# Kernel tuning notes

Measured on AMD Instinct MI355X. Metric: run time of the kernel, lower is better.

## Reference

```python
import jax, jax.numpy as jnp
import numpy as np
from functools import partial

H = 768
E = 1536
B = 4
L = 4096

def layer_norm(x, g, b, eps=1e-5):
    mu = jnp.mean(x, axis=-1, keepdims=True)
    var = jnp.mean((x - mu) ** 2, axis=-1, keepdims=True)
    return (x - mu) * jax.lax.rsqrt(var + eps) * g + b

def l2_normalize(x, eps=1e-12):
    n = jnp.sqrt(jnp.sum(x * x, axis=-1, keepdims=True))
    return x / jnp.maximum(n, eps)

def dw_conv(x, w):
    # x: [B, L, E], w: [E, 1, 3] depthwise kernel (torch Conv1d groups=E layout)
    y = jax.lax.conv_general_dilated(
        x.transpose(0, 2, 1), w, window_strides=(1,), padding=[(1, 1)],
        dimension_numbers=('NCH', 'OIH', 'NCH'), feature_group_count=E)
    return y.transpose(0, 2, 1)

def setup_inputs() -> dict:
    key = jax.random.key(0)
    ks = jax.random.split(key, 12)
    d = {}
    d['x'] = jax.random.normal(ks[0], (B, L, H), jnp.float32)
    d['ln1_g'] = jnp.ones((H,), jnp.float32)
    d['ln1_b'] = jnp.zeros((H,), jnp.float32)
    d['ln2_g'] = jnp.ones((E,), jnp.float32)
    d['ln2_b'] = jnp.zeros((E,), jnp.float32)
    d['W_in'] = 0.02 * jax.random.normal(ks[1], (3 * E, H), jnp.float32)
    d['b_in'] = jnp.zeros((3 * E,), jnp.float32)
    d['W_beta'] = jnp.zeros((E, H), jnp.float32)  # torch init: constant 0
    d['b_beta'] = jnp.ones((E,), jnp.float32)     # torch init: constant 1
    d['W_out'] = 0.02 * jax.random.normal(ks[2], (H, E), jnp.float32)
    d['b_out'] = jnp.zeros((H,), jnp.float32)
    d['W1'] = 0.02 * jax.random.normal(ks[3], (4 * H, H), jnp.float32)
    d['b1'] = jnp.zeros((4 * H,), jnp.float32)
    d['W2'] = 0.02 * jax.random.normal(ks[4], (H, 4 * H), jnp.float32)
    d['b2'] = jnp.zeros((H,), jnp.float32)
    d['conv_w'] = jax.random.normal(ks[5], (E, 1, 3), jnp.float32) / jnp.sqrt(3.0)
    d['attn_scale'] = jnp.ones((1,), jnp.float32)
    return d

def reference(x, ln1_g, ln1_b, ln2_g, ln2_b, W_in, b_in, W_beta, b_beta,
              W_out, b_out, W1, b1, W2, b2, conv_w, attn_scale):
    shortcut = x
    xn = layer_norm(x, ln1_g, ln1_b)
    qkv = xn @ W_in.T + b_in
    q, k, v = jnp.split(qkv, 3, axis=-1)
    q = jax.nn.silu(q)
    k = jax.nn.silu(k)
    v = jax.nn.gelu(v, approximate=False)
    q = l2_normalize(q) + 0.1 * k
    k = l2_normalize(k) + 0.1 * q
    q = dw_conv(q, conv_w)
    k = dw_conv(k, conv_w)
    v = dw_conv(v, conv_w)
    beta = jax.nn.sigmoid(xn @ W_beta.T + b_beta) * 0.9 + 0.1
    # initial state is zero, so v_old = 0 and v_new = beta * v (same math as torch code)
    v_new = beta * v                                   # [B, L, E]
    state = jnp.einsum('ble,blf->bef', v_new, k)       # v_new^T @ k : [B, E, E]
    out = jnp.einsum('blf,bef->ble', q, state)         # q @ state^T
    out = out * attn_scale
    out = layer_norm(out, ln2_g, ln2_b)
    out = out @ W_out.T + b_out
    x = shortcut + out
    h = layer_norm(x, ln1_g, ln1_b)
    h = jax.nn.gelu(h @ W1.T + b1, approximate=False) @ W2.T + b2
    return x + h
```

## Files before the change

### kernel.cpp

```cpp
#include <hip/hip_runtime.h>
#include <hip/hip_bf16.h>
#include <cstdint>
#include <cstddef>

using bf16_t = __hip_bfloat16;
typedef __bf16 bf16x8 __attribute__((ext_vector_type(8)));
typedef __bf16 bf16x4 __attribute__((ext_vector_type(4)));
typedef float f32x4 __attribute__((ext_vector_type(4)));

#define DEVI static __device__ __forceinline__

DEVI float b2f(bf16_t v) { return __bfloat162float(v); }

DEVI float fsigmoid(float x) { return 1.0f / (1.0f + __expf(-x)); }
DEVI float fsilu(float x) { return x * fsigmoid(x); }

DEVI float ferf(float x) {
    const float ax = fabsf(x);
    const float t = 1.0f / fmaf(0.3275911f, ax, 1.0f);
    float p = fmaf(1.061405429f, t, -1.453152027f);
    p = fmaf(p, t, 1.421413741f);
    p = fmaf(p, t, -0.284496736f);
    p = fmaf(p, t, 0.254829592f);
    p = p * t * __expf(-ax * ax);
    return copysignf(1.0f - p, x);
}
DEVI float fgelu(float x) { return 0.5f * x * (1.0f + ferf(x * 0.70710678118654752440f)); }

DEVI void g2l16(const bf16_t* g, bf16_t* l) {
    __builtin_amdgcn_global_load_lds(
        (const __attribute__((address_space(1))) void*)g,
        (__attribute__((address_space(3))) void*)l,
        16, 0, 0);
}

DEVI f32x4 mfma16(bf16x8 a, bf16x8 b, f32x4 c) {
    return __builtin_amdgcn_mfma_f32_16x16x32_bf16(a, b, c, 0, 0, 0);
}

template<int ACT, bool RESID, bool OUTBF, bool QKVSPLIT>
__global__ __launch_bounds__(256) void gemm_nt(
    const bf16_t* __restrict__ A, const bf16_t* __restrict__ B,
    void* __restrict__ Cout, const float* __restrict__ bias,
    const float* __restrict__ resid,
    float* __restrict__ normq, float* __restrict__ normk,
    int M, int N, int K, long long sA, long long sB, long long sC)
{
    __shared__ bf16_t As[128 * 64];
    __shared__ bf16_t Bs[128 * 64];

    const int t  = threadIdx.x;
    const int w  = t >> 6;
    const int ln = t & 63;
    const long long bz = blockIdx.z;
    A += bz * sA;
    B += bz * sB;
    const long long cbase = QKVSPLIT ? 0 : bz * sC;

    const int m0 = blockIdx.y * 128;
    const int n0 = blockIdx.x * 128;
    const int wm = (w >> 1) * 64;
    const int wn = (w & 1) * 64;

    f32x4 acc[4][4] = {};

    const int sr = ln >> 3;
    const int sc = (ln & 7) ^ sr;
    const bf16_t* Ap = A + (size_t)(m0 + w * 32 + sr) * K + sc * 8;
    const bf16_t* Bp = B + (size_t)(n0 + w * 32 + sr) * K + sc * 8;
    bf16_t* ldsA = &As[(w * 32) * 64];
    bf16_t* ldsB = &Bs[(w * 32) * 64];

    const int fr = ln & 15;
    const int qd = ln >> 4;
    int roA[4], roB[4];
#pragma unroll
    for (int i = 0; i < 4; ++i) {
        roA[i] = (wm + i * 16 + fr) * 64;
        roB[i] = (wn + i * 16 + fr) * 64;
    }
    const int so0 = ((qd)     ^ (fr & 7)) * 8;
    const int so1 = ((4 + qd) ^ (fr & 7)) * 8;

    for (int k0 = 0; k0 < K; k0 += 64) {
#pragma unroll
        for (int i = 0; i < 4; ++i) {
            g2l16(Ap + (size_t)(i * 8) * K, ldsA + (i * 8) * 64);
            g2l16(Bp + (size_t)(i * 8) * K, ldsB + (i * 8) * 64);
        }
        Ap += 64; Bp += 64;
        __syncthreads();

        bf16x8 af[4], bfr[4];
#pragma unroll
        for (int i = 0; i < 4; ++i) {
            af[i]  = *(const bf16x8*)&As[roA[i] + so0];
            bfr[i] = *(const bf16x8*)&Bs[roB[i] + so0];
        }
#pragma unroll
        for (int mi = 0; mi < 4; ++mi)
#pragma unroll
            for (int ni = 0; ni < 4; ++ni)
                acc[mi][ni] = mfma16(bfr[ni], af[mi], acc[mi][ni]);
#pragma unroll
        for (int i = 0; i < 4; ++i) {
            af[i]  = *(const bf16x8*)&As[roA[i] + so1];
            bfr[i] = *(const bf16x8*)&Bs[roB[i] + so1];
        }
#pragma unroll
        for (int mi = 0; mi < 4; ++mi)
#pragma unroll
            for (int ni = 0; ni < 4; ++ni)
                acc[mi][ni] = mfma16(bfr[ni], af[mi], acc[mi][ni]);
        __syncthreads();
    }

    const int rb = qd * 4;
    const int seg = QKVSPLIT ? (n0 / 1536) : 0;
    f32x4 bias4[4];
#pragma unroll
    for (int ni = 0; ni < 4; ++ni) {
        f32x4 z = {};
        bias4[ni] = bias ? *(const f32x4*)&bias[n0 + wn + ni * 16 + rb] : z;
    }
#pragma unroll
    for (int mi = 0; mi < 4; ++mi) {
        const int row = m0 + wm + mi * 16 + fr;
        float s2 = 0.f;
#pragma unroll
        for (int ni = 0; ni < 4; ++ni) {
            const int col0 = n0 + wn + ni * 16 + rb;
            f32x4 v = acc[mi][ni] + bias4[ni];
            if constexpr (ACT == 1) {
#pragma unroll
                for (int r = 0; r < 4; ++r) v[r] = fgelu(v[r]);
            }
            if constexpr (ACT == 3) {
                if (seg <= 1) {
#pragma unroll
                    for (int r = 0; r < 4; ++r) v[r] = fsilu(v[r]);
                    s2 += v[0]*v[0] + v[1]*v[1] + v[2]*v[2] + v[3]*v[3];
                } else if (seg == 2) {
#pragma unroll
                    for (int r = 0; r < 4; ++r) v[r] = fgelu(v[r]);
                } else {
#pragma unroll
                    for (int r = 0; r < 4; ++r) v[r] = fsigmoid(v[r]) * 0.9f + 0.1f;
                }
            }
            long long off;
            if constexpr (QKVSPLIT) {
                off = (long long)seg * sC + (long long)row * 1536
                    + (col0 - seg * 1536);
            } else {
                off = cbase + (long long)row * N + col0;
            }
            if constexpr (RESID) v += *(const f32x4*)&resid[off];
            if constexpr (OUTBF) {
                bf16x4 o;
#pragma unroll
                for (int r = 0; r < 4; ++r) o[r] = (__bf16)v[r];
                *(bf16x4*)((bf16_t*)Cout + off) = o;
            } else {
                *(f32x4*)((float*)Cout + off) = v;
            }
        }
        if constexpr (ACT == 3) {
            if (seg <= 1) {
                s2 += __shfl_xor(s2, 16, 64);
                s2 += __shfl_xor(s2, 32, 64);
                if (qd == 0)
                    atomicAdd((seg == 0 ? normq : normk) + row, s2);
            }
        }
    }
}

template<int ACT, bool RESID, bool OUTBF, bool QKVSPLIT>
__global__ __launch_bounds__(512) void gemm256(
    const bf16_t* __restrict__ A, const bf16_t* __restrict__ B,
    void* __restrict__ Cout, const float* __restrict__ bias,
    const float* __restrict__ resid,
    float* __restrict__ normq, float* __restrict__ normk,
    int M, int N, int K, long long sA, long long sB, long long sC)
{
    __shared__ bf16_t As[2][256 * 64];
    __shared__ bf16_t Bs[2][256 * 64];

    const int t  = threadIdx.x;
    const int w  = t >> 6;
    const int ln = t & 63;
    const int wr = w >> 2;
    const int wc = w & 3;
    const long long bz = blockIdx.z;
    A += bz * sA;
    B += bz * sB;
    const long long cbase = QKVSPLIT ? 0 : bz * sC;

    const int m0 = blockIdx.y * 256;
    const int n0 = blockIdx.x * 256;

    const int fr = ln & 15;
    const int qd = ln >> 4;
    const int sr = ln >> 3;
    const int scx = ((ln & 7) ^ sr) * 8;

    const bf16_t* gA[2];
    const bf16_t* gB[2];
    int lA[2], lB[2];
#pragma unroll
    for (int i = 0; i < 2; ++i) {
        const int b  = w * 2 + i;
        const int rA = ((b >> 3) << 7) + ((b & 7) << 3);
        const int rB = ((b >> 2) << 6) + ((b & 3) << 3);
        gA[i] = A + (size_t)(m0 + rA + sr) * K + scx;
        gB[i] = B + (size_t)(n0 + rB + sr) * K + scx;
        lA[i] = rA * 64;
        lB[i] = rB * 64;
    }
    const size_t K64 = (size_t)K * 64;
    const size_t K32 = (size_t)K * 32;
    const int NT = K >> 6;

    const int ck0 = ((qd)     ^ (fr & 7)) * 8;
    const int ck1 = ((4 + qd) ^ (fr & 7)) * 8;
    const int raB = (wr * 128 + fr) * 64;
    const int rbB = (wc * 64  + fr) * 64;

    f32x4 acc[8][4] = {};

#pragma unroll
    for (int i = 0; i < 2; ++i) {
        g2l16(gA[i],       &As[0][lA[i]]);
        g2l16(gA[i] + K64, &As[0][lA[i] + 4096]);
        g2l16(gB[i],       &Bs[0][lB[i]]);
        g2l16(gB[i] + K32, &Bs[0][lB[i] + 2048]);
    }
#pragma unroll
    for (int i = 0; i < 2; ++i) {
        g2l16(gB[i] + K32 + 64, &Bs[1][lB[i] + 2048]);
        g2l16(gA[i] + K64 + 64, &As[1][lA[i] + 4096]);
    }
    asm volatile("s_waitcnt vmcnt(4)" ::: "memory");
    __builtin_amdgcn_sched_barrier(0);
    __builtin_amdgcn_s_barrier();

    for (int u = 0; u < NT; ++u) {
        const int bs = u & 1;
        const bf16_t* Ac = As[bs];
        const bf16_t* Bc = Bs[bs];
        bf16_t* An  = As[bs ^ 1];
        bf16_t* Bn  = Bs[bs ^ 1];
        bf16_t* Acw = As[bs];
        bf16_t* Bcw = Bs[bs];
        const size_t kc1 = (size_t)(u + 1) * 64;
        const size_t kc2 = (size_t)(u + 2) * 64;
        const bool p1 = (u + 1) < NT;
        const bool p2 = (u + 2) < NT;

        bf16x8 a0[4][2], a1[4][2], bq0[2][2], bq1[2][2];

#pragma unroll
        for (int mi = 0; mi < 4; ++mi) {
            a0[mi][0] = *(const bf16x8*)&Ac[raB + mi * 1024 + ck0];
            a0[mi][1] = *(const bf16x8*)&Ac[raB + mi * 1024 + ck1];
        }
#pragma unroll
        for (int ni = 0; ni < 2; ++ni) {
            bq0[ni][0] = *(const bf16x8*)&Bc[rbB + ni * 1024 + ck0];
            bq0[ni][1] = *(const bf16x8*)&Bc[rbB + ni * 1024 + ck1];
        }
        if (p1) {
            g2l16(gA[0] + kc1, &An[lA[0]]);
            g2l16(gA[1] + kc1, &An[lA[1]]);
        }
        __builtin_amdgcn_s_barrier();
        asm volatile("s_waitcnt lgkmcnt(0)" ::: "memory");
        __builtin_amdgcn_sched_barrier(0);
        __builtin_amdgcn_s_setprio(1);
#pragma unroll
        for (int mi = 0; mi < 4; ++mi)
#pragma unroll
            for (int ni = 0; ni < 2; ++ni) {
                acc[mi][ni] = mfma16(bq0[ni][0], a0[mi][0], acc[mi][ni]);
                acc[mi][ni] = mfma16(bq0[ni][1], a0[mi][1], acc[mi][ni]);
            }
        __builtin_amdgcn_s_setprio(0);
        __builtin_amdgcn_sched_barrier(0);
        __builtin_amdgcn_s_barrier();

#pragma unroll
        for (int ni = 0; ni < 2; ++ni) {
            bq1[ni][0] = *(const bf16x8*)&Bc[rbB + 2048 + ni * 1024 + ck0];
            bq1[ni][1] = *(const bf16x8*)&Bc[rbB + 2048 + ni * 1024 + ck1];
        }
        if (p1) {
            g2l16(gB[0] + kc1, &Bn[lB[0]]);
            g2l16(gB[1] + kc1, &Bn[lB[1]]);
        }
        __builtin_amdgcn_s_barrier();
        asm volatile("s_waitcnt lgkmcnt(0)" ::: "memory");
        __builtin_amdgcn_sched_barrier(0);
        __builtin_amdgcn_s_setprio(1);
#pragma unroll
        for (int mi = 0; mi < 4; ++mi)
#pragma unroll
            for (int ni = 0; ni < 2; ++ni) {
                acc[mi][ni + 2] = mfma16(bq1[ni][0], a0[mi][0], acc[mi][ni + 2]);
                acc[mi][ni + 2] = mfma16(bq1[ni][1], a0[mi][1], acc[mi][ni + 2]);
            }
        __builtin_amdgcn_s_setprio(0);
        __builtin_amdgcn_sched_barrier(0);
        __builtin_amdgcn_s_barrier();

#pragma unroll
        for (int mi = 0; mi < 4; ++mi) {
            a1[mi][0] = *(const bf16x8*)&Ac[raB + 4096 + mi * 1024 + ck0];
            a1[mi][1] = *(const bf16x8*)&Ac[raB + 4096 + mi * 1024 + ck1];
        }
        if (p2) {
            g2l16(gB[0] + K32 + kc2, &Bcw[lB[0] + 2048]);
            g2l16(gB[1] + K32 + kc2, &Bcw[lB[1] + 2048]);
        }
        __builtin_amdgcn_s_barrier();
        asm volatile("s_waitcnt lgkmcnt(0)" ::: "memory");
        __builtin_amdgcn_sched_barrier(0);
        __builtin_amdgcn_s_setprio(1);
#pragma unroll
        for (int mi = 0; mi < 4; ++mi)
#pragma unroll
            for (int ni = 0; ni < 2; ++ni) {
                acc[mi + 4][ni] = mfma16(bq0[ni][0], a1[mi][0], acc[mi + 4][ni]);
                acc[mi + 4][ni] = mfma16(bq0[ni][1], a1[mi][1], acc[mi + 4][ni]);
            }
        __builtin_amdgcn_s_setprio(0);
        __builtin_amdgcn_sched_barrier(0);
        __builtin_amdgcn_s_barrier();

        if (p2) {
            g2l16(gA[0] + K64 + kc2, &Acw[lA[0] + 4096]);
            g2l16(gA[1] + K64 + kc2, &Acw[lA[1] + 4096]);
        }
        __builtin_amdgcn_s_setprio(1);
#pragma unroll
        for (int mi = 0; mi < 4; ++mi)
#pragma unroll
            for (int ni = 0; ni < 2; ++ni) {
                acc[mi + 4][ni + 2] = mfma16(bq1[ni][0], a1[mi][0], acc[mi + 4][ni + 2]);
                acc[mi + 4][ni + 2] = mfma16(bq1[ni][1], a1[mi][1], acc[mi + 4][ni + 2]);
            }
        __builtin_amdgcn_s_setprio(0);
        __builtin_amdgcn_sched_barrier(0);
        if (p2) asm volatile("s_waitcnt vmcnt(4)" ::: "memory");
        else    asm volatile("s_waitcnt vmcnt(0)" ::: "memory");
        __builtin_amdgcn_sched_barrier(0);
        __builtin_amdgcn_s_barrier();
    }

    const int rb = qd * 4;
    const int seg = QKVSPLIT ? (n0 / 1536) : 0;
    f32x4 bias4[4];
#pragma unroll
    for (int ni = 0; ni < 4; ++ni) {
        f32x4 z = {};
        bias4[ni] = bias ? *(const f32x4*)&bias[n0 + wc * 64 + ni * 16 + rb] : z;
    }
#pragma unroll
    for (int mi = 0; mi < 8; ++mi) {
        const int row = m0 + wr * 128 + mi * 16 + fr;
        float s2 = 0.f;
#pragma unroll
        for (int ni = 0; ni < 4; ++ni) {
            const int col0 = n0 + wc * 64 + ni * 16 + rb;
            f32x4 v = acc[mi][ni] + bias4[ni];
            if constexpr (ACT == 1) {
#pragma unroll
                for (int r = 0; r < 4; ++r) v[r] = fgelu(v[r]);
            }
            if constexpr (ACT == 3) {
                if (seg <= 1) {
#pragma unroll
                    for (int r = 0; r < 4; ++r) v[r] = fsilu(v[r]);
                    s2 += v[0]*v[0] + v[1]*v[1] + v[2]*v[2] + v[3]*v[3];
                } else if (seg == 2) {
#pragma unroll
                    for (int r = 0; r < 4; ++r) v[r] = fgelu(v[r]);
                } else {
#pragma unroll
                    for (int r = 0; r < 4; ++r) v[r] = fsigmoid(v[r]) * 0.9f + 0.1f;
                }
            }
            long long off;
            if constexpr (QKVSPLIT) {
                off = (long long)seg * sC + (long long)row * 1536
                    + (col0 - seg * 1536);
            } else {
                off = cbase + (long long)row * N + col0;
            }
            if constexpr (RESID) v += *(const f32x4*)&resid[off];
            if constexpr (OUTBF) {
                bf16x4 o;
#pragma unroll
                for (int r = 0; r < 4; ++r) o[r] = (__bf16)v[r];
                *(bf16x4*)((bf16_t*)Cout + off) = o;
            } else {
                *(f32x4*)((float*)Cout + off) = v;
            }
        }
        if constexpr (ACT == 3) {
            if (seg <= 1) {
                s2 += __shfl_xor(s2, 16, 64);
                s2 += __shfl_xor(s2, 32, 64);
                if (qd == 0)
                    atomicAdd((seg == 0 ? normq : normk) + row, s2);
            }
        }
    }
}

template<int NT>
__global__ __launch_bounds__(NT) void ln_v4(
    const float* __restrict__ x, const float* __restrict__ g,
    const float* __restrict__ b, bf16_t* __restrict__ out)
{
    constexpr int n = NT * 4;
    constexpr int NW = NT / 64;
    const int row = blockIdx.x, t = threadIdx.x;
    f32x4 v = *(const f32x4*)&x[(size_t)row * n + t * 4];
    float s  = v[0] + v[1] + v[2] + v[3];
    float ss = v[0]*v[0] + v[1]*v[1] + v[2]*v[2] + v[3]*v[3];
#pragma unroll
    for (int m = 32; m; m >>= 1) { s += __shfl_xor(s, m, 64); ss += __shfl_xor(ss, m, 64); }
    __shared__ float red[2 * NW];
    const int w = t >> 6;
    if ((t & 63) == 0) { red[w] = s; red[NW + w] = ss; }
    __syncthreads();
    s = 0.f; ss = 0.f;
#pragma unroll
    for (int i = 0; i < NW; ++i) { s += red[i]; ss += red[NW + i]; }
    const float mean = s / n;
    const float rstd = rsqrtf(ss / n - mean * mean + 1e-5f);
    const f32x4 gv = *(const f32x4*)&g[t * 4];
    const f32x4 bv = *(const f32x4*)&b[t * 4];
    bf16x4 o;
#pragma unroll
    for (int r = 0; r < 4; ++r)
        o[r] = (__bf16)((v[r] - mean) * rstd * gv[r] + bv[r]);
    *(bf16x4*)&out[(size_t)row * n + t * 4] = o;
}

__global__ __launch_bounds__(192) void ln_bf16_1536(
    const bf16_t* __restrict__ x, const float* __restrict__ g,
    const float* __restrict__ b, bf16_t* __restrict__ out,
    const float* __restrict__ scale_ptr)
{
    const int row = blockIdx.x, t = threadIdx.x;
    const float scale = scale_ptr[0];
    const bf16x8 x8 = *(const bf16x8*)&x[(size_t)row * 1536 + t * 8];
    float v[8];
    float s = 0.f, ss = 0.f;
#pragma unroll
    for (int i = 0; i < 8; ++i) {
        v[i] = (float)x8[i] * scale;
        s += v[i]; ss += v[i] * v[i];
    }
#pragma unroll
    for (int m = 32; m; m >>= 1) { s += __shfl_xor(s, m, 64); ss += __shfl_xor(ss, m, 64); }
    __shared__ float red[6];
    const int w = t >> 6;
    if ((t & 63) == 0) { red[w] = s; red[3 + w] = ss; }
    __syncthreads();
    s  = red[0] + red[1] + red[2];
    ss = red[3] + red[4] + red[5];
    const float mean = s / 1536.f;
    const float rstd = rsqrtf(ss / 1536.f - mean * mean + 1e-5f);
    const f32x4 g0 = *(const f32x4*)&g[t * 8];
    const f32x4 g1 = *(const f32x4*)&g[t * 8 + 4];
    const f32x4 b0 = *(const f32x4*)&b[t * 8];
    const f32x4 b1 = *(const f32x4*)&b[t * 8 + 4];
    bf16x8 o;
#pragma unroll
    for (int r = 0; r < 4; ++r) {
        o[r]     = (__bf16)((v[r]     - mean) * rstd * g0[r] + b0[r]);
        o[r + 4] = (__bf16)((v[r + 4] - mean) * rstd * g1[r] + b1[r]);
    }
    *(bf16x8*)&out[(size_t)row * 1536 + t * 8] = o;
}

__global__ __launch_bounds__(256) void ac_qk(
    const bf16_t* __restrict__ qs, const bf16_t* __restrict__ ks,
    const float* __restrict__ nq, const float* __restrict__ nk,
    bf16_t* __restrict__ qc, bf16_t* __restrict__ kT,
    const float* __restrict__ cw)
{
    constexpr int L = 4096, E = 1536;
    const int b = blockIdx.z;
    const int e0 = blockIdx.x * 64, l0 = blockIdx.y * 64;
    const int t = threadIdx.x;
    const int e = e0 + (t & 15) * 4;
    const int lbase = l0 + (t >> 4) * 4;
    const size_t rowL = (size_t)b * L;

    float w0[4], w1[4], w2[4];
#pragma unroll
    for (int i = 0; i < 4; ++i) {
        w0[i] = cw[(e + i) * 3 + 0];
        w1[i] = cw[(e + i) * 3 + 1];
        w2[i] = cw[(e + i) * 3 + 2];
    }

    float sq[6][4], sk[6][4];
#pragma unroll
    for (int j = 0; j < 6; ++j) {
        const int l = lbase - 1 + j;
        if (l < 0 || l >= L) {
#pragma unroll
            for (int i = 0; i < 4; ++i) { sq[j][i] = 0.f; sk[j][i] = 0.f; }
            continue;
        }
        const size_t off = (rowL + l) * E + e;
        const bf16x4 q4 = *(const bf16x4*)&qs[off];
        const bf16x4 k4 = *(const bf16x4*)&ks[off];
        const float rq = 1.0f / fmaxf(sqrtf(nq[rowL + l]), 1e-12f);
        const float rk = 1.0f / fmaxf(sqrtf(nk[rowL + l]), 1e-12f);
#pragma unroll
        for (int i = 0; i < 4; ++i) {
            const float q1 = (float)q4[i] * rq + 0.1f * (float)k4[i];
            const float k1 = (float)k4[i] * rk + 0.1f * q1;
            sq[j][i] = q1; sk[j][i] = k1;
        }
    }

#pragma unroll
    for (int j = 0; j < 4; ++j) {
        bf16x4 oq;
#pragma unroll
        for (int i = 0; i < 4; ++i)
            oq[i] = (__bf16)(w0[i] * sq[j][i] + w1[i] * sq[j + 1][i] + w2[i] * sq[j + 2][i]);
        *(bf16x4*)&qc[(rowL + lbase + j) * E + e] = oq;
    }
#pragma unroll
    for (int i = 0; i < 4; ++i) {
        bf16x4 ok;
#pragma unroll
        for (int j = 0; j < 4; ++j)
            ok[j] = (__bf16)(w0[i] * sk[j][i] + w1[i] * sk[j + 1][i] + w2[i] * sk[j + 2][i]);
        *(bf16x4*)&kT[((size_t)b * E + e + i) * L + lbase] = ok;
    }
}

__global__ __launch_bounds__(256) void ac_v(
    const bf16_t* __restrict__ vg, const bf16_t* __restrict__ beta,
    bf16_t* __restrict__ vT, const float* __restrict__ cw)
{
    constexpr int L = 4096, E = 1536;
    const int b = blockIdx.z;
    const int e0 = blockIdx.x * 64, l0 = blockIdx.y * 64;
    const int t = threadIdx.x;
    const int e = e0 + (t & 15) * 4;
    const int lbase = l0 + (t >> 4) * 4;
    const size_t rowL = (size_t)b * L;

    float w0[4], w1[4], w2[4];
#pragma unroll
    for (int i = 0; i < 4; ++i) {
        w0[i] = cw[(e + i) * 3 + 0];
        w1[i] = cw[(e + i) * 3 + 1];
        w2[i] = cw[(e + i) * 3 + 2];
    }

    float s[6][4];
#pragma unroll
    for (int j = 0; j < 6; ++j) {
        const int l = lbase - 1 + j;
        if (l < 0 || l >= L) {
#pragma unroll
            for (int i = 0; i < 4; ++i) s[j][i] = 0.f;
            continue;
        }
        const bf16x4 v4 = *(const bf16x4*)&vg[(rowL + l) * E + e];
#pragma unroll
        for (int i = 0; i < 4; ++i) s[j][i] = (float)v4[i];
    }

    float o[4][4];
#pragma unroll
    for (int j = 0; j < 4; ++j) {
        const bf16x4 b4 = *(const bf16x4*)&beta[(rowL + lbase + j) * E + e];
#pragma unroll
        for (int i = 0; i < 4; ++i)
            o[j][i] = (w0[i] * s[j][i] + w1[i] * s[j + 1][i] + w2[i] * s[j + 2][i])
                      * (float)b4[i];
    }
#pragma unroll
    for (int i = 0; i < 4; ++i) {
        bf16x4 ov;
#pragma unroll
        for (int j = 0; j < 4; ++j) ov[j] = (__bf16)o[j][i];
        *(bf16x4*)&vT[((size_t)b * E + e + i) * L + lbase] = ov;
    }
}

__global__ __launch_bounds__(256) void prep1(
    const float* __restrict__ Win, const float* __restrict__ Wbeta,
    const float* __restrict__ bin, const float* __restrict__ bbeta,
    bf16_t* __restrict__ Wcat, float* __restrict__ bcat)
{
    constexpr int nWin4 = 3 * 1536 * 768 / 4;
    constexpr int nWb4  = 1536 * 768 / 4;
    const int i = blockIdx.x * 256 + threadIdx.x;
    if (i < nWin4) {
        const f32x4 v = ((const f32x4*)Win)[i];
        bf16x4 o;
#pragma unroll
        for (int r = 0; r < 4; ++r) o[r] = (__bf16)v[r];
        ((bf16x4*)Wcat)[i] = o;
    } else if (i < nWin4 + nWb4) {
        const f32x4 v = ((const f32x4*)Wbeta)[i - nWin4];
        bf16x4 o;
#pragma unroll
        for (int r = 0; r < 4; ++r) o[r] = (__bf16)v[r];
        ((bf16x4*)Wcat)[i] = o;
    } else {
        const int j = i - nWin4 - nWb4;
        ((f32x4*)bcat)[j] = (j < 1152) ? ((const f32x4*)bin)[j]
                                       : ((const f32x4*)bbeta)[j - 1152];
    }
}

__global__ __launch_bounds__(256) void prep2(
    const float* __restrict__ Wout, const float* __restrict__ W1,
    const float* __restrict__ W2, bf16_t* __restrict__ dst)
{
    constexpr int n0 = 768 * 1536 / 4;
    constexpr int n1 = n0 + 3072 * 768 / 4;
    const int i = blockIdx.x * 256 + threadIdx.x;
    const float* src;
    int j;
    if (i < n0)      { src = Wout; j = i; }
    else if (i < n1) { src = W1;   j = i - n0; }
    else             { src = W2;   j = i - n1; }
    const f32x4 v = ((const f32x4*)src)[j];
    bf16x4 o;
#pragma unroll
    for (int r = 0; r < 4; ++r) o[r] = (__bf16)v[r];
    ((bf16x4*)dst)[i] = o;
}

__global__ void diag_ws(float* o, float v) { o[threadIdx.x] = v; }


extern "C" void kernel_launch(void* const* d_in, const int* in_sizes, int n_in,
                              void* d_out, int out_size, void* d_ws, size_t ws_size,
                              hipStream_t stream)
{
    constexpr int B = 4, L = 4096, H = 768, E = 1536;
    constexpr int T = B * L;
    constexpr size_t SEGE = (size_t)T * E;
    constexpr size_t S    = SEGE * 2;
    constexpr size_t o_bcat  = 5 * S;
    constexpr size_t o_norms = o_bcat + 6144 * 4;
    constexpr size_t WS_NEED = o_norms + (size_t)T * 8;

    const float* x       = (const float*)d_in[0];
    const float* ln1_g   = (const float*)d_in[1];
    const float* ln1_b   = (const float*)d_in[2];
    const float* ln2_g   = (const float*)d_in[3];
    const float* ln2_b   = (const float*)d_in[4];
    const float* W_in    = (const float*)d_in[5];
    const float* b_in    = (const float*)d_in[6];
    const float* W_beta  = (const float*)d_in[7];
    const float* b_beta  = (const float*)d_in[8];
    const float* W_out   = (const float*)d_in[9];
    const float* b_out   = (const float*)d_in[10];
    const float* W1      = (const float*)d_in[11];
    const float* b1      = (const float*)d_in[12];
    const float* W2      = (const float*)d_in[13];
    const float* b2      = (const float*)d_in[14];
    const float* conv_w  = (const float*)d_in[15];
    const float* attn_sc = (const float*)d_in[16];

    if (ws_size < WS_NEED) {
        diag_ws<<<1, 256, 0, stream>>>((float*)d_out,
                                       10000.0f + (float)(ws_size >> 20));
        return;
    }

    char* ws = (char*)d_ws;
    bf16_t* slotA = (bf16_t*)(ws + 0 * S);
    bf16_t* slotB = (bf16_t*)(ws + 1 * S);
    bf16_t* slotC = (bf16_t*)(ws + 2 * S);
    bf16_t* slotD = (bf16_t*)(ws + 3 * S);
    bf16_t* slotE = (bf16_t*)(ws + 4 * S);
    float*  bcat  = (float*)(ws + o_bcat);
    float*  nq    = (float*)(ws + o_norms);
    float*  nk    = nq + T;

    bf16_t* Wcat = slotE;
    bf16_t* xn   = (bf16_t*)((char*)slotE + (size_t)6144 * H * 2);

    bf16_t* vT    = slotE;
    bf16_t* kT    = slotC;
    bf16_t* qc    = slotD;
    bf16_t* state = slotA;
    bf16_t* WoutB = (bf16_t*)((char*)slotA + (size_t)20 * 1024 * 1024);
    bf16_t* W1B   = WoutB + (size_t)H * E;
    bf16_t* W2B   = W1B + (size_t)4 * H * H;
    bf16_t* attn  = slotB;
    bf16_t* ln2o  = slotE;
    float*  x2    = (float*)slotC;
    bf16_t* xn2   = slotB;
    bf16_t* h1    = slotD;

    hipMemsetAsync(nq, 0, (size_t)T * 2 * sizeof(float), stream);
    prep1<<<4614, 256, 0, stream>>>(W_in, W_beta, b_in, b_beta, Wcat, bcat);

    ln_v4<192><<<T, 192, 0, stream>>>(x, ln1_g, ln1_b, xn);

    gemm256<3, false, true, true><<<dim3(6144 / 256, T / 256, 1), 512, 0, stream>>>(
        xn, Wcat, slotA, bcat, nullptr, nq, nk, T, 6144, H, 0, 0, (long long)SEGE);

    ac_v <<<dim3(E / 64, L / 64, B), 256, 0, stream>>>(slotC, slotD, vT, conv_w);
    ac_qk<<<dim3(E / 64, L / 64, B), 256, 0, stream>>>(slotA, slotB, nq, nk, qc, kT, conv_w);

    prep2<<<5760, 256, 0, stream>>>(W_out, W1, W2, WoutB);

    gemm_nt<0, false, true, false><<<dim3(E / 128, E / 128, B), 256, 0, stream>>>(
        vT, kT, state, nullptr, nullptr, nullptr, nullptr, E, E, L,
        (long long)E * L, (long long)E * L, (long long)E * E);

    gemm256<0, false, true, false><<<dim3(E / 256, L / 256, B), 512, 0, stream>>>(
        qc, state, attn, nullptr, nullptr, nullptr, nullptr, L, E, E,
        (long long)L * E, (long long)E * E, (long long)L * E);

    ln_bf16_1536<<<T, 192, 0, stream>>>(attn, ln2_g, ln2_b, ln2o, attn_sc);

    gemm_nt<0, true, false, false><<<dim3(H / 128, T / 128, 1), 256, 0, stream>>>(
        ln2o, WoutB, x2, b_out, x, nullptr, nullptr, T, H, E, 0, 0, 0);

    ln_v4<192><<<T, 192, 0, stream>>>(x2, ln1_g, ln1_b, xn2);

    gemm256<1, false, true, false><<<dim3(4 * H / 256, T / 256, 1), 512, 0, stream>>>(
        xn2, W1B, h1, b1, nullptr, nullptr, nullptr, T, 4 * H, H, 0, 0, 0);

    gemm_nt<0, true, false, false><<<dim3(H / 128, T / 128, 1), 256, 0, stream>>>(
        h1, W2B, (float*)d_out, b2, x2, nullptr, nullptr, T, H, 4 * H, 0, 0, 0);
}
```

Baseline: 1.001 ms.

## Switch 256x256 GEMM to 32x32x16 MFMA with register-prefetched LDS fragments

Rewrites the inner loop of the large-tile GEMM to use 32x32x16 bf16 MFMA instead of 16x16x32, cutting the number of MFMA issues and LDS fragment reads per tile. It also restructures the pipeline: fragments for the next k-slice are read from LDS into registers while the current slice's MFMAs run, and global-to-LDS staging becomes a simple double buffer, one tile ahead, with one barrier per k-tile. The epilogue is remapped to the 32x32 accumulator layout and needs only one shuffle for the row-norm reduction. Risks include higher register pressure from the 16-wide accumulators and less prefetch depth, because the vmcnt(0) wait now comes every iteration.

```diff
diff --git a/kernel.cpp b/kernel.cpp
--- a/kernel.cpp
+++ b/kernel.cpp
@@ -7,6 +7,7 @@
 typedef __bf16 bf16x8 __attribute__((ext_vector_type(8)));
 typedef __bf16 bf16x4 __attribute__((ext_vector_type(4)));
 typedef float f32x4 __attribute__((ext_vector_type(4)));
+typedef float f32x16 __attribute__((ext_vector_type(16)));
 
 #define DEVI static __device__ __forceinline__
 
@@ -36,6 +37,9 @@
 
 DEVI f32x4 mfma16(bf16x8 a, bf16x8 b, f32x4 c) {
     return __builtin_amdgcn_mfma_f32_16x16x32_bf16(a, b, c, 0, 0, 0);
+}
+DEVI f32x16 mfma32(bf16x8 a, bf16x8 b, f32x16 c) {
+    return __builtin_amdgcn_mfma_f32_32x32x16_bf16(a, b, c, 0, 0, 0);
 }
 
 template<int ACT, bool RESID, bool OUTBF, bool QKVSPLIT>
@@ -200,11 +204,8 @@
     const int m0 = blockIdx.y * 256;
     const int n0 = blockIdx.x * 256;
 
-    const int fr = ln & 15;
-    const int qd = ln >> 4;
     const int sr = ln >> 3;
     const int scx = ((ln & 7) ^ sr) * 8;
-
     const bf16_t* gA[2];
     const bf16_t* gB[2];
     int lA[2], lB[2];
@@ -222,196 +223,167 @@
     const size_t K32 = (size_t)K * 32;
     const int NT = K >> 6;
 
-    const int ck0 = ((qd)     ^ (fr & 7)) * 8;
-    const int ck1 = ((4 + qd) ^ (fr & 7)) * 8;
-    const int raB = (wr * 128 + fr) * 64;
-    const int rbB = (wc * 64  + fr) * 64;
-
-    f32x4 acc[8][4] = {};
-
-#pragma unroll
-    for (int i = 0; i < 2; ++i) {
-        g2l16(gA[i],       &As[0][lA[i]]);
-        g2l16(gA[i] + K64, &As[0][lA[i] + 4096]);
-        g2l16(gB[i],       &Bs[0][lB[i]]);
-        g2l16(gB[i] + K32, &Bs[0][lB[i] + 2048]);
-    }
-#pragma unroll
-    for (int i = 0; i < 2; ++i) {
-        g2l16(gB[i] + K32 + 64, &Bs[1][lB[i] + 2048]);
-        g2l16(gA[i] + K64 + 64, &As[1][lA[i] + 4096]);
-    }
-    asm volatile("s_waitcnt vmcnt(4)" ::: "memory");
+    const int lr = ln & 31;
+    const int hh = ln >> 5;
+    const int r7 = ln & 7;
+    int rowA[4], rowB[2], sl[4];
+#pragma unroll
+    for (int mi = 0; mi < 4; ++mi) rowA[mi] = (wr * 128 + mi * 32 + lr) * 64;
+#pragma unroll
+    for (int ni = 0; ni < 2; ++ni) rowB[ni] = (wc * 64 + ni * 32 + lr) * 64;
+#pragma unroll
+    for (int ks = 0; ks < 4; ++ks) sl[ks] = ((2 * ks + hh) ^ r7) * 8;
+
+    f32x16 acc[4][2];
+#pragma unroll
+    for (int mi = 0; mi < 4; ++mi)
+#pragma unroll
+        for (int ni = 0; ni < 2; ++ni)
+#pragma unroll
+            for (int r = 0; r < 16; ++r) acc[mi][ni][r] = 0.f;
+
+    bf16x8 fA0[4], fB0[2], fA1[4], fB1[2];
+
+#define STAGE_A(dst, kc) do { \
+    g2l16(gA[0] + (kc),       &(dst)[lA[0]]); \
+    g2l16(gA[0] + K64 + (kc), &(dst)[lA[0] + 4096]); \
+    g2l16(gA[1] + (kc),       &(dst)[lA[1]]); \
+    g2l16(gA[1] + K64 + (kc), &(dst)[lA[1] + 4096]); } while (0)
+#define STAGE_B(dst, kc) do { \
+    g2l16(gB[0] + (kc),       &(dst)[lB[0]]); \
+    g2l16(gB[0] + K32 + (kc), &(dst)[lB[0] + 2048]); \
+    g2l16(gB[1] + (kc),       &(dst)[lB[1]]); \
+    g2l16(gB[1] + K32 + (kc), &(dst)[lB[1] + 2048]); } while (0)
+#define RD6(fa, fb, Ab, Bb, slot) do { \
+    fa[0] = *(const bf16x8*)&(Ab)[rowA[0] + (slot)]; \
+    fa[1] = *(const bf16x8*)&(Ab)[rowA[1] + (slot)]; \
+    fa[2] = *(const bf16x8*)&(Ab)[rowA[2] + (slot)]; \
+    fa[3] = *(const bf16x8*)&(Ab)[rowA[3] + (slot)]; \
+    fb[0] = *(const bf16x8*)&(Bb)[rowB[0] + (slot)]; \
+    fb[1] = *(const bf16x8*)&(Bb)[rowB[1] + (slot)]; } while (0)
+#define MFMA8(fa, fb) do { \
+    __builtin_amdgcn_s_setprio(1); \
+    acc[0][0] = mfma32(fb[0], fa[0], acc[0][0]); \
+    acc[0][1] = mfma32(fb[1], fa[0], acc[0][1]); \
+    acc[1][0] = mfma32(fb[0], fa[1], acc[1][0]); \
+    acc[1][1] = mfma32(fb[1], fa[1], acc[1][1]); \
+    acc[2][0] = mfma32(fb[0], fa[2], acc[2][0]); \
+    acc[2][1] = mfma32(fb[1], fa[2], acc[2][1]); \
+    acc[3][0] = mfma32(fb[0], fa[3], acc[3][0]); \
+    acc[3][1] = mfma32(fb[1], fa[3], acc[3][1]); \
+    __builtin_amdgcn_s_setprio(0); } while (0)
+
+    STAGE_A(As[0], 0);
+    STAGE_B(Bs[0], 0);
+    asm volatile("s_waitcnt vmcnt(0)" ::: "memory");
     __builtin_amdgcn_sched_barrier(0);
     __builtin_amdgcn_s_barrier();
+    __builtin_amdgcn_sched_barrier(0);
+    RD6(fA0, fB0, As[0], Bs[0], sl[0]);
 
     for (int u = 0; u < NT; ++u) {
         const int bs = u & 1;
         const bf16_t* Ac = As[bs];
         const bf16_t* Bc = Bs[bs];
-        bf16_t* An  = As[bs ^ 1];
-        bf16_t* Bn  = Bs[bs ^ 1];
-        bf16_t* Acw = As[bs];
-        bf16_t* Bcw = Bs[bs];
+        bf16_t* An = As[bs ^ 1];
+        bf16_t* Bn = Bs[bs ^ 1];
         const size_t kc1 = (size_t)(u + 1) * 64;
-        const size_t kc2 = (size_t)(u + 2) * 64;
         const bool p1 = (u + 1) < NT;
-        const bool p2 = (u + 2) < NT;
-
-        bf16x8 a0[4][2], a1[4][2], bq0[2][2], bq1[2][2];
-
-#pragma unroll
-        for (int mi = 0; mi < 4; ++mi) {
-            a0[mi][0] = *(const bf16x8*)&Ac[raB + mi * 1024 + ck0];
-            a0[mi][1] = *(const bf16x8*)&Ac[raB + mi * 1024 + ck1];
-        }
-#pragma unroll
-        for (int ni = 0; ni < 2; ++ni) {
-            bq0[ni][0] = *(const bf16x8*)&Bc[rbB + ni * 1024 + ck0];
-            bq0[ni][1] = *(const bf16x8*)&Bc[rbB + ni * 1024 + ck1];
-        }
-        if (p1) {
-            g2l16(gA[0] + kc1, &An[lA[0]]);
-            g2l16(gA[1] + kc1, &An[lA[1]]);
-        }
-        __builtin_amdgcn_s_barrier();
+
+        if (p1) STAGE_A(An, kc1);
+        RD6(fA1, fB1, Ac, Bc, sl[1]);
+        asm volatile("s_waitcnt lgkmcnt(6)" ::: "memory");
+        __builtin_amdgcn_sched_barrier(0);
+        MFMA8(fA0, fB0);
+
+        if (p1) STAGE_B(Bn, kc1);
+        RD6(fA0, fB0, Ac, Bc, sl[2]);
+        asm volatile("s_waitcnt lgkmcnt(6)" ::: "memory");
+        __builtin_amdgcn_sched_barrier(0);
+        MFMA8(fA1, fB1);
+
+        RD6(fA1, fB1, Ac, Bc, sl[3]);
+        asm volatile("s_waitcnt lgkmcnt(6)" ::: "memory");
+        __builtin_amdgcn_sched_barrier(0);
+        MFMA8(fA0, fB0);
+
         asm volatile("s_waitcnt lgkmcnt(0)" ::: "memory");
         __builtin_amdgcn_sched_barrier(0);
-        __builtin_amdgcn_s_setprio(1);
-#pragma unroll
-        for (int mi = 0; mi < 4; ++mi)
-#pragma unroll
-            for (int ni = 0; ni < 2; ++ni) {
-                acc[mi][ni] = mfma16(bq0[ni][0], a0[mi][0], acc[mi][ni]);
-                acc[mi][ni] = mfma16(bq0[ni][1], a0[mi][1], acc[mi][ni]);
-            }
-        __builtin_amdgcn_s_setprio(0);
+        asm volatile("s_waitcnt vmcnt(0)" ::: "memory");
         __builtin_amdgcn_sched_barrier(0);
         __builtin_amdgcn_s_barrier();
-
+        __builtin_amdgcn_sched_barrier(0);
+        if (p1) RD6(fA0, fB0, An, Bn, sl[0]);
+        MFMA8(fA1, fB1);
+    }
+#undef STAGE_A
+#undef STAGE_B
+#undef RD6
+#undef MFMA8
+
+    const int h4 = hh * 4;
+    const int seg = QKVSPLIT ? (n0 / 1536) : 0;
+    f32x4 bias4[2][4];
+#pragma unroll
+    for (int ni = 0; ni < 2; ++ni)
+#pragma unroll
+        for (int g = 0; g < 4; ++g) {
+            f32x4 z = {};
+            bias4[ni][g] = bias
+                ? *(const f32x4*)&bias[n0 + wc * 64 + ni * 32 + g * 8 + h4] : z;
+        }
+#pragma unroll
+    for (int mi = 0; mi < 4; ++mi) {
+        const int row = m0 + wr * 128 + mi * 32 + lr;
+        float s2 = 0.f;
 #pragma unroll
         for (int ni = 0; ni < 2; ++ni) {
-            bq1[ni][0] = *(const bf16x8*)&Bc[rbB + 2048 + ni * 1024 + ck0];
-            bq1[ni][1] = *(const bf16x8*)&Bc[rbB + 2048 + ni * 1024 + ck1];
-        }
-        if (p1) {
-            g2l16(gB[0] + kc1, &Bn[lB[0]]);
-            g2l16(gB[1] + kc1, &Bn[lB[1]]);
-        }
-        __builtin_amdgcn_s_barrier();
-        asm volatile("s_waitcnt lgkmcnt(0)" ::: "memory");
-        __builtin_amdgcn_sched_barrier(0);
-        __builtin_amdgcn_s_setprio(1);
-#pragma unroll
-        for (int mi = 0; mi < 4; ++mi)
-#pragma unroll
-            for (int ni = 0; ni < 2; ++ni) {
-                acc[mi][ni + 2] = mfma16(bq1[ni][0], a0[mi][0], acc[mi][ni + 2]);
-                acc[mi][ni + 2] = mfma16(bq1[ni][1], a0[mi][1], acc[mi][ni + 2]);
-            }
-        __builtin_amdgcn_s_setprio(0);
-        __builtin_amdgcn_sched_barrier(0);
-        __builtin_amdgcn_s_barrier();
-
-#pragma unroll
-        for (int mi = 0; mi < 4; ++mi) {
-            a1[mi][0] = *(const bf16x8*)&Ac[raB + 4096 + mi * 1024 + ck0];
-            a1[mi][1] = *(const bf16x8*)&Ac[raB + 4096 + mi * 1024 + ck1];
-        }
-        if (p2) {
-            g2l16(gB[0] + K32 + kc2, &Bcw[lB[0] + 2048]);
-            g2l16(gB[1] + K32 + kc2, &Bcw[lB[1] + 2048]);
-        }
-        __builtin_amdgcn_s_barrier();
-        asm volatile("s_waitcnt lgkmcnt(0)" ::: "memory");
-        __builtin_amdgcn_sched_barrier(0);
-        __builtin_amdgcn_s_setprio(1);
-#pragma unroll
-        for (int mi = 0; mi < 4; ++mi)
-#pragma unroll
-            for (int ni = 0; ni < 2; ++ni) {
-                acc[mi + 4][ni] = mfma16(bq0[ni][0], a1[mi][0], acc[mi + 4][ni]);
-                acc[mi + 4][ni] = mfma16(bq0[ni][1], a1[mi][1], acc[mi + 4][ni]);
-            }
-        __builtin_amdgcn_s_setprio(0);
-        __builtin_amdgcn_sched_barrier(0);
-        __builtin_amdgcn_s_barrier();
-
-        if (p2) {
-            g2l16(gA[0] + K64 + kc2, &Acw[lA[0] + 4096]);
-            g2l16(gA[1] + K64 + kc2, &Acw[lA[1] + 4096]);
-        }
-        __builtin_amdgcn_s_setprio(1);
-#pragma unroll
-        for (int mi = 0; mi < 4; ++mi)
-#pragma unroll
-            for (int ni = 0; ni < 2; ++ni) {
-                acc[mi + 4][ni + 2] = mfma16(bq1[ni][0], a1[mi][0], acc[mi + 4][ni + 2]);
-                acc[mi + 4][ni + 2] = mfma16(bq1[ni][1], a1[mi][1], acc[mi + 4][ni + 2]);
-            }
-        __builtin_amdgcn_s_setprio(0);
-        __builtin_amdgcn_sched_barrier(0);
-        if (p2) asm volatile("s_waitcnt vmcnt(4)" ::: "memory");
-        else    asm volatile("s_waitcnt vmcnt(0)" ::: "memory");
-        __builtin_amdgcn_sched_barrier(0);
-        __builtin_amdgcn_s_barrier();
-    }
-
-    const int rb = qd * 4;
-    const int seg = QKVSPLIT ? (n0 / 1536) : 0;
-    f32x4 bias4[4];
-#pragma unroll
-    for (int ni = 0; ni < 4; ++ni) {
-        f32x4 z = {};
-        bias4[ni] = bias ? *(const f32x4*)&bias[n0 + wc * 64 + ni * 16 + rb] : z;
-    }
-#pragma unroll
-    for (int mi = 0; mi < 8; ++mi) {
-        const int row = m0 + wr * 128 + mi * 16 + fr;
-        float s2 = 0.f;
-#pragma unroll
-        for (int ni = 0; ni < 4; ++ni) {
-            const int col0 = n0 + wc * 64 + ni * 16 + rb;
-            f32x4 v = acc[mi][ni] + bias4[ni];
-            if constexpr (ACT == 1) {
-#pragma unroll
-                for (int r = 0; r < 4; ++r) v[r] = fgelu(v[r]);
-            }
-            if constexpr (ACT == 3) {
-                if (seg <= 1) {
-#pragma unroll
-                    for (int r = 0; r < 4; ++r) v[r] = fsilu(v[r]);
-                    s2 += v[0]*v[0] + v[1]*v[1] + v[2]*v[2] + v[3]*v[3];
-                } else if (seg == 2) {
+#pragma unroll
+            for (int g = 0; g < 4; ++g) {
+                const int col0 = n0 + wc * 64 + ni * 32 + g * 8 + h4;
+                f32x4 v;
+#pragma unroll
+                for (int r = 0; r < 4; ++r) v[r] = acc[mi][ni][g * 4 + r];
+                v += bias4[ni][g];
+                if constexpr (ACT == 1) {
 #pragma unroll
                     for (int r = 0; r < 4; ++r) v[r] = fgelu(v[r]);
+                }
+                if constexpr (ACT == 3) {
+                    if (seg <= 1) {
+#pragma unroll
+                        for (int r = 0; r < 4; ++r) v[r] = fsilu(v[r]);
+                        s2 += v[0]*v[0] + v[1]*v[1] + v[2]*v[2] + v[3]*v[3];
+                    } else if (seg == 2) {
+#pragma unroll
+                        for (int r = 0; r < 4; ++r) v[r] = fgelu(v[r]);
+                    } else {
+#pragma unroll
+                        for (int r = 0; r < 4; ++r) v[r] = fsigmoid(v[r]) * 0.9f + 0.1f;
+                    }
+                }
+                long long off;
+                if constexpr (QKVSPLIT) {
+                    off = (long long)seg * sC + (long long)row * 1536
+                        + (col0 - seg * 1536);
                 } else {
-#pragma unroll
-                    for (int r = 0; r < 4; ++r) v[r] = fsigmoid(v[r]) * 0.9f + 0.1f;
+                    off = cbase + (long long)row * N + col0;
+                }
+                if constexpr (RESID) v += *(const f32x4*)&resid[off];
+                if constexpr (OUTBF) {
+                    bf16x4 o;
+#pragma unroll
+                    for (int r = 0; r < 4; ++r) o[r] = (__bf16)v[r];
+                    *(bf16x4*)((bf16_t*)Cout + off) = o;
+                } else {
+                    *(f32x4*)((float*)Cout + off) = v;
                 }
             }
-            long long off;
-            if constexpr (QKVSPLIT) {
-                off = (long long)seg * sC + (long long)row * 1536
-                    + (col0 - seg * 1536);
-            } else {
-                off = cbase + (long long)row * N + col0;
-            }
-            if constexpr (RESID) v += *(const f32x4*)&resid[off];
-            if constexpr (OUTBF) {
-                bf16x4 o;
-#pragma unroll
-                for (int r = 0; r < 4; ++r) o[r] = (__bf16)v[r];
-                *(bf16x4*)((bf16_t*)Cout + off) = o;
-            } else {
-                *(f32x4*)((float*)Cout + off) = v;
-            }
         }
         if constexpr (ACT == 3) {
             if (seg <= 1) {
-                s2 += __shfl_xor(s2, 16, 64);
                 s2 += __shfl_xor(s2, 32, 64);
-                if (qd == 0)
+                if (hh == 0)
                     atomicAdd((seg == 0 ? normq : normk) + row, s2);
             }
         }
```

Measured after the change: 1.056 ms. 1.05x slower.

## Single-buffer GEMM LDS tiles with quarter-staged in-place refills

Applied to the files above, without the earlier changes.

Replaces the double-buffered 256x64 A/B shared-memory tiles with a single buffer. Each quarter of the tile is refilled for the next K step as soon as its last reader finishes, with vmcnt waits and barriers placed around each refill. This halves LDS use (128KB to 64KB), which could allow more blocks per CU or less LDS pressure. In exchange the prefetch distance is shorter, there are more waits on global loads, and the loop depends on exact barrier ordering to stay correct.

```diff
diff --git a/kernel.cpp b/kernel.cpp
--- a/kernel.cpp
+++ b/kernel.cpp
@@ -184,8 +184,8 @@
     float* __restrict__ normq, float* __restrict__ normk,
     int M, int N, int K, long long sA, long long sB, long long sC)
 {
-    __shared__ bf16_t As[2][256 * 64];
-    __shared__ bf16_t Bs[2][256 * 64];
+    __shared__ bf16_t As[256 * 64];
+    __shared__ bf16_t Bs[256 * 64];
 
     const int t  = threadIdx.x;
     const int w  = t >> 6;
@@ -200,11 +200,8 @@
     const int m0 = blockIdx.y * 256;
     const int n0 = blockIdx.x * 256;
 
-    const int fr = ln & 15;
-    const int qd = ln >> 4;
     const int sr = ln >> 3;
     const int scx = ((ln & 7) ^ sr) * 8;
-
     const bf16_t* gA[2];
     const bf16_t* gB[2];
     int lA[2], lB[2];
@@ -222,6 +219,8 @@
     const size_t K32 = (size_t)K * 32;
     const int NT = K >> 6;
 
+    const int fr = ln & 15;
+    const int qd = ln >> 4;
     const int ck0 = ((qd)     ^ (fr & 7)) * 8;
     const int ck1 = ((4 + qd) ^ (fr & 7)) * 8;
     const int raB = (wr * 128 + fr) * 64;
@@ -229,52 +228,40 @@
 
     f32x4 acc[8][4] = {};
 
-#pragma unroll
-    for (int i = 0; i < 2; ++i) {
-        g2l16(gA[i],       &As[0][lA[i]]);
-        g2l16(gA[i] + K64, &As[0][lA[i] + 4096]);
-        g2l16(gB[i],       &Bs[0][lB[i]]);
-        g2l16(gB[i] + K32, &Bs[0][lB[i] + 2048]);
-    }
-#pragma unroll
-    for (int i = 0; i < 2; ++i) {
-        g2l16(gB[i] + K32 + 64, &Bs[1][lB[i] + 2048]);
-        g2l16(gA[i] + K64 + 64, &As[1][lA[i] + 4096]);
-    }
-    asm volatile("s_waitcnt vmcnt(4)" ::: "memory");
-    __builtin_amdgcn_sched_barrier(0);
-    __builtin_amdgcn_s_barrier();
+#define STAGE_A0(kc) do { g2l16(gA[0] + (kc), &As[lA[0]]); \
+                          g2l16(gA[1] + (kc), &As[lA[1]]); } while (0)
+#define STAGE_A1(kc) do { g2l16(gA[0] + K64 + (kc), &As[lA[0] + 4096]); \
+                          g2l16(gA[1] + K64 + (kc), &As[lA[1] + 4096]); } while (0)
+#define STAGE_B0(kc) do { g2l16(gB[0] + (kc), &Bs[lB[0]]); \
+                          g2l16(gB[1] + (kc), &Bs[lB[1]]); } while (0)
+#define STAGE_B1(kc) do { g2l16(gB[0] + K32 + (kc), &Bs[lB[0] + 2048]); \
+                          g2l16(gB[1] + K32 + (kc), &Bs[lB[1] + 2048]); } while (0)
+
+    STAGE_A0(0);
+    STAGE_B0(0);
+    STAGE_B1(0);
+    STAGE_A1(0);
+
+    bf16x8 a0[4][2], a1[4][2], bq0[2][2], bq1[2][2];
 
     for (int u = 0; u < NT; ++u) {
-        const int bs = u & 1;
-        const bf16_t* Ac = As[bs];
-        const bf16_t* Bc = Bs[bs];
-        bf16_t* An  = As[bs ^ 1];
-        bf16_t* Bn  = Bs[bs ^ 1];
-        bf16_t* Acw = As[bs];
-        bf16_t* Bcw = Bs[bs];
         const size_t kc1 = (size_t)(u + 1) * 64;
-        const size_t kc2 = (size_t)(u + 2) * 64;
         const bool p1 = (u + 1) < NT;
-        const bool p2 = (u + 2) < NT;
-
-        bf16x8 a0[4][2], a1[4][2], bq0[2][2], bq1[2][2];
-
+
+        asm volatile("s_waitcnt vmcnt(4)" ::: "memory");
+        __builtin_amdgcn_sched_barrier(0);
+        __builtin_amdgcn_s_barrier();
+        __builtin_amdgcn_sched_barrier(0);
 #pragma unroll
         for (int mi = 0; mi < 4; ++mi) {
-            a0[mi][0] = *(const bf16x8*)&Ac[raB + mi * 1024 + ck0];
-            a0[mi][1] = *(const bf16x8*)&Ac[raB + mi * 1024 + ck1];
+            a0[mi][0] = *(const bf16x8*)&As[raB + mi * 1024 + ck0];
+            a0[mi][1] = *(const bf16x8*)&As[raB + mi * 1024 + ck1];
         }
 #pragma unroll
         for (int ni = 0; ni < 2; ++ni) {
-            bq0[ni][0] = *(const bf16x8*)&Bc[rbB + ni * 1024 + ck0];
-            bq0[ni][1] = *(const bf16x8*)&Bc[rbB + ni * 1024 + ck1];
-        }
-        if (p1) {
-            g2l16(gA[0] + kc1, &An[lA[0]]);
-            g2l16(gA[1] + kc1, &An[lA[1]]);
-        }
-        __builtin_amdgcn_s_barrier();
+            bq0[ni][0] = *(const bf16x8*)&Bs[rbB + ni * 1024 + ck0];
+            bq0[ni][1] = *(const bf16x8*)&Bs[rbB + ni * 1024 + ck1];
+        }
         asm volatile("s_waitcnt lgkmcnt(0)" ::: "memory");
         __builtin_amdgcn_sched_barrier(0);
         __builtin_amdgcn_s_setprio(1);
@@ -287,18 +274,17 @@
             }
         __builtin_amdgcn_s_setprio(0);
         __builtin_amdgcn_sched_barrier(0);
+
+        asm volatile("s_waitcnt vmcnt(2)" ::: "memory");
+        __builtin_amdgcn_sched_barrier(0);
         __builtin_amdgcn_s_barrier();
-
+        __builtin_amdgcn_sched_barrier(0);
+        if (p1) STAGE_A0(kc1);
 #pragma unroll
         for (int ni = 0; ni < 2; ++ni) {
-            bq1[ni][0] = *(const bf16x8*)&Bc[rbB + 2048 + ni * 1024 + ck0];
-            bq1[ni][1] = *(const bf16x8*)&Bc[rbB + 2048 + ni * 1024 + ck1];
-        }
-        if (p1) {
-            g2l16(gB[0] + kc1, &Bn[lB[0]]);
-            g2l16(gB[1] + kc1, &Bn[lB[1]]);
-        }
-        __builtin_amdgcn_s_barrier();
+            bq1[ni][0] = *(const bf16x8*)&Bs[rbB + 2048 + ni * 1024 + ck0];
+            bq1[ni][1] = *(const bf16x8*)&Bs[rbB + 2048 + ni * 1024 + ck1];
+        }
         asm volatile("s_waitcnt lgkmcnt(0)" ::: "memory");
         __builtin_amdgcn_sched_barrier(0);
         __builtin_amdgcn_s_setprio(1);
@@ -311,18 +297,18 @@
             }
         __builtin_amdgcn_s_setprio(0);
         __builtin_amdgcn_sched_barrier(0);
+
+        if (p1) asm volatile("s_waitcnt vmcnt(2)" ::: "memory");
+        else    asm volatile("s_waitcnt vmcnt(0)" ::: "memory");
+        __builtin_amdgcn_sched_barrier(0);
         __builtin_amdgcn_s_barrier();
-
+        __builtin_amdgcn_sched_barrier(0);
+        if (p1) { STAGE_B0(kc1); STAGE_B1(kc1); }
 #pragma unroll
         for (int mi = 0; mi < 4; ++mi) {
-            a1[mi][0] = *(const bf16x8*)&Ac[raB + 4096 + mi * 1024 + ck0];
-            a1[mi][1] = *(const bf16x8*)&Ac[raB + 4096 + mi * 1024 + ck1];
-        }
-        if (p2) {
-            g2l16(gB[0] + K32 + kc2, &Bcw[lB[0] + 2048]);
-            g2l16(gB[1] + K32 + kc2, &Bcw[lB[1] + 2048]);
-        }
-        __builtin_amdgcn_s_barrier();
+            a1[mi][0] = *(const bf16x8*)&As[raB + 4096 + mi * 1024 + ck0];
+            a1[mi][1] = *(const bf16x8*)&As[raB + 4096 + mi * 1024 + ck1];
+        }
         asm volatile("s_waitcnt lgkmcnt(0)" ::: "memory");
         __builtin_amdgcn_sched_barrier(0);
         __builtin_amdgcn_s_setprio(1);
@@ -335,12 +321,10 @@
             }
         __builtin_amdgcn_s_setprio(0);
         __builtin_amdgcn_sched_barrier(0);
+
         __builtin_amdgcn_s_barrier();
-
-        if (p2) {
-            g2l16(gA[0] + K64 + kc2, &Acw[lA[0] + 4096]);
-            g2l16(gA[1] + K64 + kc2, &Acw[lA[1] + 4096]);
-        }
+        __builtin_amdgcn_sched_barrier(0);
+        if (p1) STAGE_A1(kc1);
         __builtin_amdgcn_s_setprio(1);
 #pragma unroll
         for (int mi = 0; mi < 4; ++mi)
@@ -351,11 +335,11 @@
             }
         __builtin_amdgcn_s_setprio(0);
         __builtin_amdgcn_sched_barrier(0);
-        if (p2) asm volatile("s_waitcnt vmcnt(4)" ::: "memory");
-        else    asm volatile("s_waitcnt vmcnt(0)" ::: "memory");
-        __builtin_amdgcn_sched_barrier(0);
-        __builtin_amdgcn_s_barrier();
-    }
+    }
+#undef STAGE_A0
+#undef STAGE_A1
+#undef STAGE_B0
+#undef STAGE_B1
 
     const int rb = qd * 4;
     const int seg = QKVSPLIT ? (n0 / 1536) : 0;
```

Measured after the change: 1.150 ms. 1.15x slower.
